# Kernel optimization log

Hardware: AMD Instinct MI355X
Metric: run time of the kernel (lower is better)

Reference implementation:

```python
import jax, jax.numpy as jnp
import numpy as np

D_MODEL = 1024
NUM_HEADS = 16
D_K = D_MODEL // NUM_HEADS


def setup_inputs() -> dict:
    key = jax.random.key(0)
    ks = jax.random.split(key, 12)
    B, S, D = 2, 2048, D_MODEL
    s = 1.0 / np.sqrt(D)
    inp = {
        "Q": jax.random.normal(ks[0], (B, S, D), jnp.float32),
        "K": jax.random.normal(ks[1], (B, S, D), jnp.float32),
        "V": jax.random.normal(ks[2], (B, S, D), jnp.float32),
        "Wq": jax.random.normal(ks[3], (D, D), jnp.float32) * s,
        "bq": jax.random.normal(ks[4], (D,), jnp.float32) * s,
        "Wk": jax.random.normal(ks[5], (D, D), jnp.float32) * s,
        "bk": jax.random.normal(ks[6], (D,), jnp.float32) * s,
        "Wv": jax.random.normal(ks[7], (D, D), jnp.float32) * s,
        "bv": jax.random.normal(ks[8], (D,), jnp.float32) * s,
        "Wo": jax.random.normal(ks[9], (D, D), jnp.float32) * s,
        "bo": jax.random.normal(ks[10], (D,), jnp.float32) * s,
    }
    return inp


def _split_heads(x, B, S):
    # [B, S, D] -> [B, H, S, d_k]
    return x.reshape(B, S, NUM_HEADS, D_K).transpose(0, 2, 1, 3)


def reference(Q, K, V, Wq, bq, Wk, bk, Wv, bv, Wo, bo):
    B, S, D = Q.shape
    # torch nn.Linear: y = x @ W.T + b
    q = _split_heads(Q @ Wq.T + bq, B, S)
    k = _split_heads(K @ Wk.T + bk, B, S)
    v = _split_heads(V @ Wv.T + bv, B, S)
    scale = 1.0 / np.sqrt(D_K).astype(np.float32)
    # [B, H, S, S] attention scores (materialized, as in the original)
    scores = jnp.einsum('bhqd,bhkd->bhqk', q, k) * scale
    probs = jax.nn.softmax(scores, axis=-1)
    out = jnp.einsum('bhqk,bhkd->bhqd', probs, v)
    out = out.transpose(0, 2, 1, 3).reshape(B, S, D)
    return out @ Wo.T + bo
```

## Files before the change

### kernel.cpp

```cpp
#include <hip/hip_runtime.h>
#include <hip/hip_bf16.h>

#define S_LEN   2048
#define NHEADS  16
#define DKH     64
#define DMODEL  1024
#define NBATCH  2

typedef __bf16 bf16x8 __attribute__((ext_vector_type(8)));
typedef __bf16 bf16x4 __attribute__((ext_vector_type(4)));
typedef float  f32x4  __attribute__((ext_vector_type(4)));

typedef __attribute__((address_space(3))) void       lds_void;
typedef const __attribute__((address_space(1))) void glob_void;

__device__ __forceinline__ void glds16(const void* g, void* l) {
    __builtin_amdgcn_global_load_lds((glob_void*)g, (lds_void*)l, 16, 0, 0);
}

struct CvtArgs {
    const float* src[7];
    __bf16*      dst[7];
    int          n[7];
};

__global__ __launch_bounds__(256)
void cvt_all_k(CvtArgs a)
{
    const int t = blockIdx.y;
    const size_t i = ((size_t)blockIdx.x * 256 + threadIdx.x) * 8;
    if ((int)i >= a.n[t]) return;
    const float* s = a.src[t];
    f32x4 lo = *(const f32x4*)(s + i);
    f32x4 hi = *(const f32x4*)(s + i + 4);
    bf16x8 r;
#pragma unroll
    for (int k = 0; k < 4; ++k) { r[k] = (__bf16)lo[k]; r[4 + k] = (__bf16)hi[k]; }
    *(bf16x8*)(a.dst[t] + i) = r;
}

__device__ __forceinline__ void gemm_core(
    const __bf16* __restrict__ A, const __bf16* __restrict__ W,
    int m0, int n0, int K,
    __bf16* AsB, __bf16* WsB, f32x4 acc[4][4])
{
    const int tid  = threadIdx.x;
    const int lane = tid & 63;
    const int wv   = tid >> 6;
    const int l15  = lane & 15;
    const int quad = lane >> 4;
    const int wm   = wv >> 1;
    const int wn   = wv & 1;
    const int grow = lane >> 2;
    const int gcol = (lane & 3) * 8;

    const __bf16* ag0 = A + (size_t)(m0 + wv * 32 + grow) * K + gcol;
    const __bf16* ag1 = ag0 + (size_t)16 * K;
    const __bf16* wg0 = W + (size_t)(n0 + wv * 32 + grow) * K + gcol;
    const __bf16* wg1 = wg0 + (size_t)16 * K;
    char* al0 = (char*)(AsB + (wv * 32) * 32);
    char* al1 = (char*)(AsB + (wv * 32 + 16) * 32);
    char* wl0 = (char*)(WsB + (wv * 32) * 32);
    char* wl1 = (char*)(WsB + (wv * 32 + 16) * 32);

    glds16(ag0, al0); glds16(ag1, al1);
    glds16(wg0, wl0); glds16(wg1, wl1);
    __syncthreads();

    int cb = 0;
    for (int k0 = 0;;) {
        const int nk = k0 + 32;
        if (nk < K) {
            const int nb = cb ^ 8192;
            glds16(ag0 + nk, al0 + nb); glds16(ag1 + nk, al1 + nb);
            glds16(wg0 + nk, wl0 + nb); glds16(wg1 + nk, wl1 + nb);
        }
        const __bf16* Ac = (const __bf16*)((const char*)AsB + cb);
        const __bf16* Wc = (const __bf16*)((const char*)WsB + cb);
        bf16x8 af[4], wf[4];
#pragma unroll
        for (int i = 0; i < 4; ++i)
            af[i] = *(const bf16x8*)(Ac + (size_t)(wm * 64 + i * 16 + l15) * 32 + quad * 8);
#pragma unroll
        for (int j = 0; j < 4; ++j)
            wf[j] = *(const bf16x8*)(Wc + (size_t)(wn * 64 + j * 16 + l15) * 32 + quad * 8);
#pragma unroll
        for (int i = 0; i < 4; ++i)
#pragma unroll
            for (int j = 0; j < 4; ++j)
                acc[i][j] = __builtin_amdgcn_mfma_f32_16x16x32_bf16(af[i], wf[j], acc[i][j], 0, 0, 0);

        if (nk >= K) break;
        __syncthreads();
        cb ^= 8192;
        k0 = nk;
    }
}

struct GArgs {
    const __bf16* A[3];
    const __bf16* W[3];
    const float*  bias[3];
    __bf16*       out[3];
};

__global__ __launch_bounds__(256)
void gemm_qkv(GArgs g, int z_off)
{
    __shared__ __align__(16) __bf16 As[2][128][32];
    __shared__ __align__(16) __bf16 Ws[2][128][32];

    const int fid = blockIdx.x;
    const int z   = (fid >> 8) + z_off;
    const int f8  = fid & 255;
    int m0, n0;
    if (z == 2) { m0 = (f8 & 7) * 128;  n0 = (f8 >> 3) * 128; }
    else        { m0 = (f8 & 31) * 128; n0 = (f8 >> 5) * 128; }

    f32x4 acc[4][4];
#pragma unroll
    for (int i = 0; i < 4; ++i)
#pragma unroll
        for (int j = 0; j < 4; ++j) acc[i][j] = (f32x4){0.f, 0.f, 0.f, 0.f};

    gemm_core(g.A[z], g.W[z], m0, n0, DMODEL, &As[0][0][0], &Ws[0][0][0], acc);

    const int lane = threadIdx.x & 63;
    const int wv   = threadIdx.x >> 6;
    const int l15  = lane & 15;
    const int quad = lane >> 4;
    const int wm   = wv >> 1;
    const int wn   = wv & 1;
    const float* bias = g.bias[z];
    __bf16* out = g.out[z];
    const float oscale = (z == 0) ? 0.125f * 1.44269504088896f : 1.0f;

#pragma unroll
    for (int j = 0; j < 4; ++j) {
        const int col = n0 + wn * 64 + j * 16 + l15;
        const float bcol = (z == 2) ? 0.f : bias[col];
#pragma unroll
        for (int i = 0; i < 4; ++i) {
#pragma unroll
            for (int r = 0; r < 4; ++r) {
                const int row = m0 + wm * 64 + i * 16 + quad * 4 + r;
                size_t idx;
                float v = acc[i][j][r];
                if (z == 2) {
                    const int h = row >> 6, d = row & (DKH - 1);
                    const int b = col >> 11, s = col & (S_LEN - 1);
                    v += bias[row];
                    idx = ((size_t)(b * NHEADS + h) * DKH + d) * S_LEN + s;
                } else {
                    const int b = row >> 11, s = row & (S_LEN - 1);
                    const int h = col >> 6, d = col & (DKH - 1);
                    v = (v + bcol) * oscale;
                    idx = ((size_t)(b * NHEADS + h) * S_LEN + s) * DKH + d;
                }
                out[idx] = (__bf16)v;
            }
        }
    }
}

__global__ __launch_bounds__(256)
void gemm_out(const __bf16* __restrict__ A, const __bf16* __restrict__ W,
              const float* __restrict__ bias, float* __restrict__ out)
{
    __shared__ __align__(16) __bf16 As[2][128][32];
    __shared__ __align__(16) __bf16 Ws[2][128][32];

    const int fid = blockIdx.x;
    const int m0 = (fid & 31) * 128;
    const int n0 = (fid >> 5) * 128;

    f32x4 acc[4][4];
#pragma unroll
    for (int i = 0; i < 4; ++i)
#pragma unroll
        for (int j = 0; j < 4; ++j) acc[i][j] = (f32x4){0.f, 0.f, 0.f, 0.f};

    gemm_core(A, W, m0, n0, DMODEL, &As[0][0][0], &Ws[0][0][0], acc);

    const int lane = threadIdx.x & 63;
    const int wv   = threadIdx.x >> 6;
    const int l15  = lane & 15;
    const int quad = lane >> 4;
    const int wm   = wv >> 1;
    const int wn   = wv & 1;

#pragma unroll
    for (int j = 0; j < 4; ++j) {
        const int col = n0 + wn * 64 + j * 16 + l15;
        const float bv = bias[col];
#pragma unroll
        for (int i = 0; i < 4; ++i)
#pragma unroll
            for (int r = 0; r < 4; ++r) {
                const int row = m0 + wm * 64 + i * 16 + quad * 4 + r;
                out[(size_t)row * DMODEL + col] = acc[i][j][r] + bv;
            }
    }
}

__global__ __launch_bounds__(256, 2)
void attn_k(const __bf16* __restrict__ Qh, const __bf16* __restrict__ Kh,
            const __bf16* __restrict__ VhT, __bf16* __restrict__ out)
{
    __shared__ __align__(16) __bf16 Ks[128][72];
    __shared__ __align__(16) __bf16 Vs[64][136];

    const int tid  = threadIdx.x;
    const int lane = tid & 63;
    const int wv   = tid >> 6;
    const int l15  = lane & 15;
    const int quad = lane >> 4;

    const int fid = blockIdx.x;
    const int x  = fid & 7;
    const int j  = fid >> 3;
    const int bh = x * 4 + (j & 3);
    const int q0 = (j >> 2) * 128;
    const int b  = bh >> 4;
    const int h  = bh & (NHEADS - 1);

    const __bf16* Q  = Qh  + (size_t)bh * S_LEN * DKH;
    const __bf16* Kp = Kh  + (size_t)bh * S_LEN * DKH;
    const __bf16* Vt = VhT + (size_t)bh * DKH * S_LEN;

    const int qrA = q0 + wv * 32 + l15;
    const int qrB = qrA + 16;
    const bf16x8 qa0 = *(const bf16x8*)(Q + (size_t)qrA * DKH + quad * 8);
    const bf16x8 qa1 = *(const bf16x8*)(Q + (size_t)qrA * DKH + quad * 8 + 32);
    const bf16x8 qb0 = *(const bf16x8*)(Q + (size_t)qrB * DKH + quad * 8);
    const bf16x8 qb1 = *(const bf16x8*)(Q + (size_t)qrB * DKH + quad * 8 + 32);

    const int krow = tid >> 1;
    const int kc0  = (tid & 1) * 32;
    const int vrow = tid >> 2;
    const int vc0  = (tid & 3) * 32;
    const __bf16* kst = Kp + (size_t)krow * DKH   + kc0;
    const __bf16* vst = Vt + (size_t)vrow * S_LEN + vc0;

    f32x4 oA[4], oB[4];
#pragma unroll
    for (int jj = 0; jj < 4; ++jj) {
        oA[jj] = (f32x4){0.f, 0.f, 0.f, 0.f};
        oB[jj] = (f32x4){0.f, 0.f, 0.f, 0.f};
    }
    float laccA = 0.f, laccB = 0.f;

    bf16x8 kr[4], vr[4];
#pragma unroll
    for (int i = 0; i < 4; ++i) kr[i] = *(const bf16x8*)(kst + 8 * i);
#pragma unroll
    for (int i = 0; i < 4; ++i) vr[i] = *(const bf16x8*)(vst + 8 * i);

    for (int kt = 0; kt < S_LEN; kt += 128) {
        __syncthreads();
#pragma unroll
        for (int i = 0; i < 4; ++i) *(bf16x8*)&Ks[krow][kc0 + 8 * i] = kr[i];
#pragma unroll
        for (int i = 0; i < 4; ++i) *(bf16x8*)&Vs[vrow][vc0 + 8 * i] = vr[i];
        __syncthreads();
        if (kt + 128 < S_LEN) {
#pragma unroll
            for (int i = 0; i < 4; ++i)
                kr[i] = *(const bf16x8*)(kst + (size_t)(kt + 128) * DKH + 8 * i);
#pragma unroll
            for (int i = 0; i < 4; ++i)
                vr[i] = *(const bf16x8*)(vst + kt + 128 + 8 * i);
        }

#pragma unroll
        for (int ht = 0; ht < 2; ++ht) {
            __builtin_amdgcn_s_setprio(1);
            float pA[4][4], pB[4][4];
#pragma unroll
            for (int n = 0; n < 4; ++n) {
                bf16x8 kA = *(const bf16x8*)&Ks[ht * 64 + n * 16 + l15][quad * 8];
                bf16x8 kB = *(const bf16x8*)&Ks[ht * 64 + n * 16 + l15][quad * 8 + 32];
                f32x4 sA = {0.f, 0.f, 0.f, 0.f};
                f32x4 sB = {0.f, 0.f, 0.f, 0.f};
                sA = __builtin_amdgcn_mfma_f32_16x16x32_bf16(kA, qa0, sA, 0, 0, 0);
                sB = __builtin_amdgcn_mfma_f32_16x16x32_bf16(kA, qb0, sB, 0, 0, 0);
                sA = __builtin_amdgcn_mfma_f32_16x16x32_bf16(kB, qa1, sA, 0, 0, 0);
                sB = __builtin_amdgcn_mfma_f32_16x16x32_bf16(kB, qb1, sB, 0, 0, 0);
#pragma unroll
                for (int r = 0; r < 4; ++r) {
                    pA[n][r] = __builtin_amdgcn_exp2f(sA[r]);
                    pB[n][r] = __builtin_amdgcn_exp2f(sB[r]);
                }
            }
#pragma unroll
            for (int n = 0; n < 4; ++n)
#pragma unroll
                for (int r = 0; r < 4; ++r) { laccA += pA[n][r]; laccB += pB[n][r]; }

#pragma unroll
            for (int t = 0; t < 2; ++t) {
                bf16x8 pfA, pfB;
#pragma unroll
                for (int jj = 0; jj < 4; ++jj) {
                    pfA[jj]     = (__bf16)pA[2 * t][jj];
                    pfA[4 + jj] = (__bf16)pA[2 * t + 1][jj];
                    pfB[jj]     = (__bf16)pB[2 * t][jj];
                    pfB[4 + jj] = (__bf16)pB[2 * t + 1][jj];
                }
#pragma unroll
                for (int jt = 0; jt < 4; ++jt) {
                    bf16x4 v0 = *(const bf16x4*)&Vs[jt * 16 + l15][ht * 64 + t * 32 + quad * 4];
                    bf16x4 v1 = *(const bf16x4*)&Vs[jt * 16 + l15][ht * 64 + t * 32 + 16 + quad * 4];
                    bf16x8 vf;
#pragma unroll
                    for (int jj = 0; jj < 4; ++jj) { vf[jj] = v0[jj]; vf[4 + jj] = v1[jj]; }
                    oA[jt] = __builtin_amdgcn_mfma_f32_16x16x32_bf16(vf, pfA, oA[jt], 0, 0, 0);
                    oB[jt] = __builtin_amdgcn_mfma_f32_16x16x32_bf16(vf, pfB, oB[jt], 0, 0, 0);
                }
            }
            __builtin_amdgcn_s_setprio(0);
        }
    }

    laccA += __shfl_xor(laccA, 16);
    laccA += __shfl_xor(laccA, 32);
    laccB += __shfl_xor(laccB, 16);
    laccB += __shfl_xor(laccB, 32);
    const float invA = 1.0f / laccA;
    const float invB = 1.0f / laccB;

    __bf16* opA = out + ((size_t)b * S_LEN + qrA) * DMODEL + h * DKH;
    __bf16* opB = out + ((size_t)b * S_LEN + qrB) * DMODEL + h * DKH;
#pragma unroll
    for (int jt = 0; jt < 4; ++jt) {
        bf16x4 tA, tB;
#pragma unroll
        for (int r = 0; r < 4; ++r) {
            tA[r] = (__bf16)(oA[jt][r] * invA);
            tB[r] = (__bf16)(oB[jt][r] * invB);
        }
        *(bf16x4*)(opA + jt * 16 + quad * 4) = tA;
        *(bf16x4*)(opB + jt * 16 + quad * 4) = tB;
    }
}

extern "C" void kernel_launch(void* const* d_in, const int* in_sizes, int n_in,
                              void* d_out, int out_size, void* d_ws, size_t ws_size,
                              hipStream_t stream) {
    const float* Qi = (const float*)d_in[0];
    const float* Ki = (const float*)d_in[1];
    const float* Vi = (const float*)d_in[2];
    const float* Wq = (const float*)d_in[3];
    const float* bq = (const float*)d_in[4];
    const float* Wk = (const float*)d_in[5];
    const float* bk = (const float*)d_in[6];
    const float* Wv = (const float*)d_in[7];
    const float* bv = (const float*)d_in[8];
    const float* Wo = (const float*)d_in[9];
    const float* bo = (const float*)d_in[10];
    float* out = (float*)d_out;

    const int M = NBATCH * S_LEN;
    const size_t NW = (size_t)DMODEL * DMODEL;
    const size_t NE = (size_t)M * DMODEL;

    __bf16* w_bf   = (__bf16*)d_ws;
    __bf16* Qin_bf = w_bf + 4 * NW;
    __bf16* Kin_bf = Qin_bf + NE;
    __bf16* Vin_bf = Kin_bf + NE;
    __bf16* q_ws   = Vin_bf + NE;
    __bf16* k_ws   = q_ws + NE;
    const bool big = ws_size >= ((size_t)56 << 20);
    __bf16* vT_ws   = big ? (k_ws + NE) : Kin_bf;
    __bf16* attn_ws = Qin_bf;
    __bf16* wq_bf = w_bf, *wk_bf = w_bf + NW, *wv_bf = w_bf + 2 * NW, *wo_bf = w_bf + 3 * NW;

    CvtArgs ca;
    ca.src[0] = Wq; ca.src[1] = Wk; ca.src[2] = Wv; ca.src[3] = Wo;
    ca.src[4] = Qi; ca.src[5] = Ki; ca.src[6] = Vi;
    ca.dst[0] = wq_bf; ca.dst[1] = wk_bf; ca.dst[2] = wv_bf; ca.dst[3] = wo_bf;
    ca.dst[4] = Qin_bf; ca.dst[5] = Kin_bf; ca.dst[6] = Vin_bf;
    for (int t = 0; t < 4; ++t) ca.n[t] = (int)NW;
    for (int t = 4; t < 7; ++t) ca.n[t] = (int)NE;
    cvt_all_k<<<dim3(2048, 7), 256, 0, stream>>>(ca);

    GArgs g;
    g.A[0] = Qin_bf; g.W[0] = wq_bf; g.bias[0] = bq; g.out[0] = q_ws;
    g.A[1] = Kin_bf; g.W[1] = wk_bf; g.bias[1] = bk; g.out[1] = k_ws;
    g.A[2] = wv_bf;  g.W[2] = Vin_bf; g.bias[2] = bv; g.out[2] = vT_ws;
    if (big) {
        gemm_qkv<<<dim3(768), 256, 0, stream>>>(g, 0);
    } else {
        gemm_qkv<<<dim3(512), 256, 0, stream>>>(g, 0);
        gemm_qkv<<<dim3(256), 256, 0, stream>>>(g, 2);
    }

    attn_k<<<dim3(512), dim3(256), 0, stream>>>(q_ws, k_ws, vT_ws, attn_ws);

    gemm_out<<<dim3(256), 256, 0, stream>>>(attn_ws, wo_bf, bo, out);
}
```

Before: 220.9 us.

## Triple-buffer GEMM LDS pipeline and remap blocks across XCDs

The GEMM core moves from a double-buffered LDS loop with a full __syncthreads to a three-stage ring buffer. It prefetches two tiles ahead and uses explicit vmcnt waits plus a raw s_barrier, so global-to-LDS loads overlap more MFMA work. Both GEMM kernels also remap block IDs so that consecutive logical tiles land on the same XCD chiplet, which should improve L2 reuse. The extra buffer raises LDS use per block from 32KB to 48KB, which may reduce occupancy, and the hand-written waitcnt logic is fragile.

```diff
diff --git a/kernel.cpp b/kernel.cpp
--- a/kernel.cpp
+++ b/kernel.cpp
@@ -58,25 +58,33 @@
     const __bf16* ag1 = ag0 + (size_t)16 * K;
     const __bf16* wg0 = W + (size_t)(n0 + wv * 32 + grow) * K + gcol;
     const __bf16* wg1 = wg0 + (size_t)16 * K;
-    char* al0 = (char*)(AsB + (wv * 32) * 32);
-    char* al1 = (char*)(AsB + (wv * 32 + 16) * 32);
-    char* wl0 = (char*)(WsB + (wv * 32) * 32);
-    char* wl1 = (char*)(WsB + (wv * 32 + 16) * 32);
-
-    glds16(ag0, al0); glds16(ag1, al1);
-    glds16(wg0, wl0); glds16(wg1, wl1);
-    __syncthreads();
-
-    int cb = 0;
-    for (int k0 = 0;;) {
-        const int nk = k0 + 32;
-        if (nk < K) {
-            const int nb = cb ^ 8192;
-            glds16(ag0 + nk, al0 + nb); glds16(ag1 + nk, al1 + nb);
-            glds16(wg0 + nk, wl0 + nb); glds16(wg1 + nk, wl1 + nb);
+    char* al0 = (char*)AsB + (wv * 32) * 64;
+    char* al1 = al0 + 16 * 64;
+    char* wl0 = (char*)WsB + (wv * 32) * 64;
+    char* wl1 = wl0 + 16 * 64;
+
+    const int NT = K >> 5;
+    glds16(ag0,      al0);        glds16(ag1,      al1);
+    glds16(wg0,      wl0);        glds16(wg1,      wl1);
+    glds16(ag0 + 32, al0 + 8192); glds16(ag1 + 32, al1 + 8192);
+    glds16(wg0 + 32, wl0 + 8192); glds16(wg1 + 32, wl1 + 8192);
+
+    int bt = 0;
+    for (int t = 0; t < NT; ++t) {
+        if (t + 1 < NT) asm volatile("s_waitcnt vmcnt(4)" ::: "memory");
+        else            asm volatile("s_waitcnt vmcnt(0)" ::: "memory");
+        __builtin_amdgcn_s_barrier();
+        __builtin_amdgcn_sched_barrier(0);
+
+        if (t + 2 < NT) {
+            int nb = bt + 16384; if (nb >= 24576) nb -= 24576;
+            const int kk = (t + 2) * 32;
+            glds16(ag0 + kk, al0 + nb); glds16(ag1 + kk, al1 + nb);
+            glds16(wg0 + kk, wl0 + nb); glds16(wg1 + kk, wl1 + nb);
         }
-        const __bf16* Ac = (const __bf16*)((const char*)AsB + cb);
-        const __bf16* Wc = (const __bf16*)((const char*)WsB + cb);
+
+        const __bf16* Ac = (const __bf16*)((const char*)AsB + bt);
+        const __bf16* Wc = (const __bf16*)((const char*)WsB + bt);
         bf16x8 af[4], wf[4];
 #pragma unroll
         for (int i = 0; i < 4; ++i)
@@ -90,10 +98,7 @@
             for (int j = 0; j < 4; ++j)
                 acc[i][j] = __builtin_amdgcn_mfma_f32_16x16x32_bf16(af[i], wf[j], acc[i][j], 0, 0, 0);
 
-        if (nk >= K) break;
-        __syncthreads();
-        cb ^= 8192;
-        k0 = nk;
+        bt += 8192; if (bt == 24576) bt = 0;
     }
 }
 
@@ -107,12 +112,14 @@
 __global__ __launch_bounds__(256)
 void gemm_qkv(GArgs g, int z_off)
 {
-    __shared__ __align__(16) __bf16 As[2][128][32];
-    __shared__ __align__(16) __bf16 Ws[2][128][32];
-
-    const int fid = blockIdx.x;
-    const int z   = (fid >> 8) + z_off;
-    const int f8  = fid & 255;
+    __shared__ __align__(16) __bf16 As[3][128][32];
+    __shared__ __align__(16) __bf16 Ws[3][128][32];
+
+    const int fid   = blockIdx.x;
+    const int chunk = gridDim.x >> 3;
+    const int lid   = (fid & 7) * chunk + (fid >> 3);
+    const int z   = (lid >> 8) + z_off;
+    const int f8  = lid & 255;
     int m0, n0;
     if (z == 2) { m0 = (f8 & 7) * 128;  n0 = (f8 >> 3) * 128; }
     else        { m0 = (f8 & 31) * 128; n0 = (f8 >> 5) * 128; }
@@ -167,12 +174,14 @@
 void gemm_out(const __bf16* __restrict__ A, const __bf16* __restrict__ W,
               const float* __restrict__ bias, float* __restrict__ out)
 {
-    __shared__ __align__(16) __bf16 As[2][128][32];
-    __shared__ __align__(16) __bf16 Ws[2][128][32];
-
-    const int fid = blockIdx.x;
-    const int m0 = (fid & 31) * 128;
-    const int n0 = (fid >> 5) * 128;
+    __shared__ __align__(16) __bf16 As[3][128][32];
+    __shared__ __align__(16) __bf16 Ws[3][128][32];
+
+    const int fid   = blockIdx.x;
+    const int chunk = gridDim.x >> 3;
+    const int lid   = (fid & 7) * chunk + (fid >> 3);
+    const int m0 = (lid & 31) * 128;
+    const int n0 = (lid >> 5) * 128;
 
     f32x4 acc[4][4];
 #pragma unroll
```

Measured after the change: 256.4 us. +16.1%, slower.
